# Optimization experiments

Measured on AMD Instinct MI355X. Metric: run time of the kernel, lower is better.

Reference implementation:

```python
import jax, jax.numpy as jnp
import numpy as np

ITERS = 3
K = 64
C = 256


def setup_inputs() -> dict:
    key = jax.random.key(0)
    ks = jax.random.split(key, 6)
    N, H, W = 2, 60, 60
    cnn_feature = jax.random.normal(ks[0], (N, C, H, W), dtype=jnp.float32)
    points = jax.random.normal(ks[1], (N, 3, H, W), dtype=jnp.float32)
    # torch Linear params: weight (out, in), bias (out,)
    s1 = 1.0 / np.sqrt(C)
    s2 = 1.0 / np.sqrt(2 * C)
    mlp_w = jax.random.uniform(ks[2], (C, C), jnp.float32, -s1, s1)
    mlp_b = jax.random.uniform(ks[3], (C,), jnp.float32, -s1, s1)
    rnn_w = jax.random.uniform(ks[4], (C, 2 * C), jnp.float32, -s2, s2)
    rnn_b = jax.random.uniform(ks[5], (C,), jnp.float32, -s2, s2)
    return {"cnn_feature": cnn_feature, "points": points, "mlp_w": mlp_w,
            "mlp_b": mlp_b, "rnn_w": rnn_w, "rnn_b": rnn_b}


def reference(cnn_feature, points, mlp_w, mlp_b, rnn_w, rnn_b):
    N, Cc, H, W = cnn_feature.shape
    HW = H * W
    pts = points.reshape(N, 3, HW).transpose(0, 2, 1)  # (N, HW, 3)
    # pairwise Euclidean distances via Gram matrix
    r = jnp.einsum('nid,njd->nij', pts, pts)           # (N, HW, HW)
    sq = jnp.einsum('nid,nid->ni', pts, pts)           # (N, HW)
    D = jnp.sqrt(jnp.maximum(sq[:, :, None] + sq[:, None, :] - 2.0 * r, 0.0))
    _, idx = jax.lax.top_k(-D, K)                      # (N, HW, K) smallest distances

    h = cnn_feature.transpose(0, 2, 3, 1).reshape(N, HW, Cc)  # (N, HW, C)
    bidx = jnp.arange(N)[:, None, None]
    for _ in range(ITERS):
        nb = h[bidx, idx]                              # (N, HW, K, C) gather
        nb = jax.nn.relu(jnp.einsum('nskc,dc->nskd', nb, mlp_w) + mlp_b)
        message = nb.mean(axis=2)                      # (N, HW, C)
        nh = jnp.concatenate([h, message], axis=-1)    # (N, HW, 2C)
        h = jax.nn.relu(jnp.einsum('nsc,dc->nsd', nh, rnn_w) + rnn_b)
    h = h.reshape(N, H, W, Cc).transpose(0, 3, 1, 2)   # (N, C, H, W)
    return jnp.concatenate([cnn_feature, h], axis=1)   # (N, 2C, H, W)
```

## Files before the change

### kernel.cpp

```cpp
#include <hip/hip_runtime.h>
#include <stdint.h>

typedef unsigned int uint;
typedef unsigned long long ull;

#define HW 3600
#define NBATCH 2
#define CDIM 256
#define KNN 64
#define M_REAL 7200
#define PADM 7232
#define QPB 8

#define TKB 900
#define IHB 904
#define SUB 64

using short8  = __attribute__((ext_vector_type(8))) short;
using floatx4 = __attribute__((ext_vector_type(4))) float;

__device__ inline unsigned short f2bf(float f) {
    uint u = __float_as_uint(f);
    uint r = u + 0x7FFFu + ((u >> 16) & 1u);
    return (unsigned short)(r >> 16);
}
__device__ inline float bf2f(unsigned short b) {
    return __uint_as_float(((uint)b) << 16);
}

__device__ inline void wave_select(uint* hist, uint* s_bin, uint* s_want,
                                   int lane, uint want) {
    uint h0 = hist[4 * lane + 0], h1 = hist[4 * lane + 1];
    uint h2 = hist[4 * lane + 2], h3 = hist[4 * lane + 3];
    hist[4 * lane + 0] = 0; hist[4 * lane + 1] = 0;
    hist[4 * lane + 2] = 0; hist[4 * lane + 3] = 0;
    uint c4 = h0 + h1 + h2 + h3;
    uint v = c4;
    #pragma unroll
    for (int off = 1; off < 64; off <<= 1) {
        uint o = __shfl_up(v, off, 64);
        if (lane >= off) v += o;
    }
    uint below = v - c4;
    if (below < want && want <= v) {
        uint b = 4 * lane, c = below;
        if (c + h0 < want) { c += h0; b = 4 * lane + 1;
            if (c + h1 < want) { c += h1; b = 4 * lane + 2;
                if (c + h2 < want) { c += h2; b = 4 * lane + 3; } } }
        *s_bin = b;
        *s_want = want - c;
    }
}

union MegaSmem {
    struct {
        float4 pts[HW];
        uint hist[QPB][256];
        uint s_bin[QPB], s_want[QPB], s_cnt[QPB];
    } tk;
    struct { float tile[2][32][33]; } ih;
};

__global__ __launch_bounds__(512) void mega_kernel(
    const float* __restrict__ points, int* __restrict__ idx_out,
    const float* __restrict__ cnn, unsigned short* __restrict__ NH,
    float* __restrict__ out,
    const float* __restrict__ mw, const float* __restrict__ rw,
    unsigned short* __restrict__ mo, unsigned short* __restrict__ ro) {
    __shared__ MegaSmem sm;
    const int blk = blockIdx.x;

    if (blk >= TKB + IHB) {
        int i0 = (blk - TKB - IHB) * 2048 + threadIdx.x * 4;
        float4 v = *(const float4*)&rw[i0];
        uint2 p;
        p.x = (uint)f2bf(v.x) | ((uint)f2bf(v.y) << 16);
        p.y = (uint)f2bf(v.z) | ((uint)f2bf(v.w) << 16);
        *(uint2*)&ro[i0] = p;
        if (i0 < 65536) {
            float4 m = *(const float4*)&mw[i0];
            p.x = (uint)f2bf(m.x) | ((uint)f2bf(m.y) << 16);
            p.y = (uint)f2bf(m.z) | ((uint)f2bf(m.w) << 16);
            *(uint2*)&mo[i0] = p;
        }
        return;
    }

    if (blk >= TKB) {
        const int b = blk - TKB;
        const int n = b / 452;
        const int r = b - n * 452;
        const int hw0 = (r % 113) * 32;
        const int c0 = (r / 113) * 64 + ((threadIdx.x >> 8) << 5);
        const int t8 = threadIdx.x & 255;
        const int tx = t8 & 31;
        const int ty = t8 >> 5;
        float (*tile)[33] = sm.ih.tile[threadIdx.x >> 8];
        const float* __restrict__ src = cnn + (size_t)n * CDIM * HW;
        #pragma unroll
        for (int rr = 0; rr < 4; ++rr) {
            int cc = ty + rr * 8;
            int hw = hw0 + tx;
            if (hw < HW) {
                float v = src[(size_t)(c0 + cc) * HW + hw];
                tile[cc][tx] = v;
                out[(size_t)n * (2 * CDIM * HW) + (size_t)(c0 + cc) * HW + hw] = v;
            }
        }
        __syncthreads();
        #pragma unroll
        for (int rr = 0; rr < 4; ++rr) {
            int hh = ty + rr * 8;
            int hw = hw0 + hh;
            if (hw < HW)
                NH[(size_t)(n * HW + hw) * 512 + c0 + tx] = f2bf(tile[tx][hh]);
        }
        return;
    }

    const int wv = threadIdx.x >> 6;
    const int lane = threadIdx.x & 63;
    const int q = blk * QPB + wv;
    const int n = (blk * QPB) / HW;
    const int i = q - n * HW;

    const float* __restrict__ px = points + (size_t)n * 3 * HW;
    const float* __restrict__ py = px + HW;
    const float* __restrict__ pz = py + HW;

    for (int j = threadIdx.x; j < HW; j += 512)
        sm.tk.pts[j] = make_float4(px[j], py[j], pz[j], 0.0f);
    sm.tk.hist[wv][4 * lane + 0] = 0; sm.tk.hist[wv][4 * lane + 1] = 0;
    sm.tk.hist[wv][4 * lane + 2] = 0; sm.tk.hist[wv][4 * lane + 3] = 0;
    if (lane == 0) sm.tk.s_cnt[wv] = 0;
    __syncthreads();

    float4 pq = sm.tk.pts[i];
    const float xi = pq.x, yi = pq.y, zi = pq.z;
    const float sqi = xi * xi + yi * yi + zi * zi;

    uint qp[29];
    #pragma unroll
    for (int s = 0; s < 57; ++s) {
        int j = (s << 6) + lane;
        uint q16 = 0xFFFFu;
        if (j < HW) {
            float4 p = sm.tk.pts[j];
            float d2 = fmaxf(sqi + (p.x * p.x + p.y * p.y + p.z * p.z)
                             - 2.0f * (xi * p.x + yi * p.y + zi * p.z), 0.0f);
            q16 = (uint)fminf(d2 * 1024.0f, 65535.0f);
        }
        if (s & 1) qp[s >> 1] |= q16 << 16; else qp[s >> 1] = q16;
    }
    #define Q16(s) ((qp[(s) >> 1] >> (((s) & 1) << 4)) & 0xFFFFu)

    #pragma unroll
    for (int s = 0; s < 57; ++s) {
        int j = (s << 6) + lane;
        if (j < HW) atomicAdd(&sm.tk.hist[wv][Q16(s) >> 8], 1u);
    }
    __syncthreads();
    wave_select(&sm.tk.hist[wv][0], &sm.tk.s_bin[wv], &sm.tk.s_want[wv], lane, KNN);
    __syncthreads();
    const uint qT8 = sm.tk.s_bin[wv];
    const uint want2 = sm.tk.s_want[wv];
    __syncthreads();

    #pragma unroll
    for (int s = 0; s < 57; ++s) {
        int j = (s << 6) + lane;
        uint k = Q16(s);
        if (j < HW && (k >> 8) == qT8)
            atomicAdd(&sm.tk.hist[wv][k & 255u], 1u);
    }
    __syncthreads();
    wave_select(&sm.tk.hist[wv][0], &sm.tk.s_bin[wv], &sm.tk.s_want[wv], lane, want2);
    __syncthreads();
    const uint qT16 = (qT8 << 8) | sm.tk.s_bin[wv];
    const uint want3 = sm.tk.s_want[wv];

    #pragma unroll
    for (int s = 0; s < 57; ++s) {
        if (Q16(s) < qT16) {
            uint pos = atomicAdd(&sm.tk.s_cnt[wv], 1u);
            if (pos < KNN) idx_out[(size_t)q * KNN + pos] = (s << 6) + lane;
        }
    }

    ull cand[4] = {~0ULL, ~0ULL, ~0ULL, ~0ULL};
    int ncand = 0;
    #pragma unroll
    for (int s = 0; s < 57; ++s) {
        int j = (s << 6) + lane;
        if (j < HW && Q16(s) == qT16) {
            float4 p = sm.tk.pts[j];
            float d2 = fmaxf(sqi + (p.x * p.x + p.y * p.y + p.z * p.z)
                             - 2.0f * (xi * p.x + yi * p.y + zi * p.z), 0.0f);
            ull key = ((ull)__float_as_uint(d2) << 32) | (uint)j;
            if      (ncand == 0) cand[0] = key;
            else if (ncand == 1) cand[1] = key;
            else if (ncand == 2) cand[2] = key;
            else if (ncand == 3) cand[3] = key;
            ++ncand;
        }
    }
    const int base = KNN - (int)want3;
    if (__ballot(ncand > 4) == 0ULL) {
        for (int r = 0; r < (int)want3; ++r) {
            ull best = cand[0] < cand[1] ? cand[0] : cand[1];
            ull b23  = cand[2] < cand[3] ? cand[2] : cand[3];
            best = best < b23 ? best : b23;
            #pragma unroll
            for (int off = 1; off < 64; off <<= 1) {
                ull o = __shfl_xor(best, off, 64);
                if (o < best) best = o;
            }
            if (lane == 0) idx_out[(size_t)q * KNN + base + r] = (int)(uint)best;
            #pragma unroll
            for (int c = 0; c < 4; ++c)
                if (cand[c] == best) cand[c] = ~0ULL;
        }
    } else {
        ull used = 0ULL;
        for (int r = 0; r < (int)want3; ++r) {
            ull best = ~0ULL;
            #pragma unroll
            for (int s = 0; s < 57; ++s) {
                int j = (s << 6) + lane;
                if (j < HW && Q16(s) == qT16 && !((used >> s) & 1ULL)) {
                    float4 p = sm.tk.pts[j];
                    float d2 = fmaxf(sqi + (p.x * p.x + p.y * p.y + p.z * p.z)
                                     - 2.0f * (xi * p.x + yi * p.y + zi * p.z), 0.0f);
                    ull key = ((ull)__float_as_uint(d2) << 32) | (uint)j;
                    if (key < best) best = key;
                }
            }
            #pragma unroll
            for (int off = 1; off < 64; off <<= 1) {
                ull o = __shfl_xor(best, off, 64);
                if (o < best) best = o;
            }
            uint jw = (uint)best;
            if (lane == 0) idx_out[(size_t)q * KNN + base + r] = (int)jw;
            if ((int)(jw & 63u) == lane) used |= 1ULL << (jw >> 6);
        }
    }
    #undef Q16
}

#define LDKP 264
__global__ __launch_bounds__(256) void gemm_mfma(
    const unsigned short* __restrict__ A, int lda,
    const unsigned short* __restrict__ W, int ldw,
    const float* __restrict__ bias,
    unsigned short* __restrict__ Cb, int ldc,
    float* __restrict__ outp, int mode, int Kk) {
    __shared__ __align__(16) unsigned short As[64 * LDKP];
    __shared__ __align__(16) unsigned short Bs[64 * LDKP];
    const int m0 = blockIdx.x * 64;
    const int n0 = blockIdx.y * 64;
    const int tid = threadIdx.x;
    const int lane = tid & 63;
    const int w = tid >> 6;
    const int wm = (w & 1) * 32;
    const int wn = (w >> 1) * 32;
    const int l15 = lane & 15;
    const int qd = lane >> 4;

    floatx4 acc[2][2];
    #pragma unroll
    for (int a = 0; a < 2; ++a)
        #pragma unroll
        for (int b = 0; b < 2; ++b)
            acc[a][b] = (floatx4){0.f, 0.f, 0.f, 0.f};

    const int srow = tid >> 5;
    const int scol = (tid & 31) * 8;

    for (int k0 = 0; k0 < Kk; k0 += 256) {
        if (k0) __syncthreads();
        #pragma unroll
        for (int r8 = 0; r8 < 8; ++r8) {
            int row = r8 * 8 + srow;
            *(float4*)&As[row * LDKP + scol] =
                *(const float4*)&A[(size_t)(m0 + row) * lda + k0 + scol];
            *(float4*)&Bs[row * LDKP + scol] =
                *(const float4*)&W[(size_t)(n0 + row) * ldw + k0 + scol];
        }
        __syncthreads();
        #pragma unroll
        for (int ks = 0; ks < 256; ks += 32) {
            short8 a0 = *(const short8*)&As[(wm + l15) * LDKP + ks + qd * 8];
            short8 a1 = *(const short8*)&As[(wm + 16 + l15) * LDKP + ks + qd * 8];
            short8 b0 = *(const short8*)&Bs[(wn + l15) * LDKP + ks + qd * 8];
            short8 b1 = *(const short8*)&Bs[(wn + 16 + l15) * LDKP + ks + qd * 8];
            acc[0][0] = __builtin_amdgcn_mfma_f32_16x16x32_bf16(a0, b0, acc[0][0], 0, 0, 0);
            acc[0][1] = __builtin_amdgcn_mfma_f32_16x16x32_bf16(a0, b1, acc[0][1], 0, 0, 0);
            acc[1][0] = __builtin_amdgcn_mfma_f32_16x16x32_bf16(a1, b0, acc[1][0], 0, 0, 0);
            acc[1][1] = __builtin_amdgcn_mfma_f32_16x16x32_bf16(a1, b1, acc[1][1], 0, 0, 0);
        }
    }

    #pragma unroll
    for (int in = 0; in < 2; ++in) {
        int col = n0 + wn + in * 16 + l15;
        float bv = bias[col];
        #pragma unroll
        for (int im = 0; im < 2; ++im) {
            int mb = m0 + wm + im * 16 + qd * 4;
            if (mode == 0) {
                #pragma unroll
                for (int r = 0; r < 4; ++r)
                    Cb[(size_t)(mb + r) * ldc + col] =
                        f2bf(fmaxf(acc[im][in][r] + bv, 0.0f));
            } else if (mb < M_REAL) {
                int nb = mb / HW;
                int hw = mb - nb * HW;
                float4 o;
                o.x = fmaxf(acc[im][in][0] + bv, 0.0f);
                o.y = fmaxf(acc[im][in][1] + bv, 0.0f);
                o.z = fmaxf(acc[im][in][2] + bv, 0.0f);
                o.w = fmaxf(acc[im][in][3] + bv, 0.0f);
                *(float4*)&outp[(size_t)nb * (2 * CDIM * HW)
                                + (size_t)(CDIM + col) * HW + hw] = o;
            }
        }
    }
}

__global__ __launch_bounds__(256) void gather_mean(const unsigned short* __restrict__ T,
                                                   const int* __restrict__ idx,
                                                   unsigned short* __restrict__ NH) {
    const int q = blockIdx.x * 4 + (threadIdx.x >> 6);
    const int lane = threadIdx.x & 63;
    const int n = q / HW;
    const int half = lane >> 5;
    const int c8 = (lane & 31) * 8;

    const int nbrL = idx[(size_t)q * KNN + lane];
    float acc[8] = {0, 0, 0, 0, 0, 0, 0, 0};
    #pragma unroll 4
    for (int it = 0; it < 32; ++it) {
        int k = 2 * it + half;
        int j = __shfl(nbrL, k, 64);
        j = min(max(j, 0), HW - 1);
        int r = n * HW + j;
        uint4 v = *(const uint4*)&T[(size_t)r * CDIM + c8];
        acc[0] += bf2f((unsigned short)(v.x & 0xFFFFu));
        acc[1] += bf2f((unsigned short)(v.x >> 16));
        acc[2] += bf2f((unsigned short)(v.y & 0xFFFFu));
        acc[3] += bf2f((unsigned short)(v.y >> 16));
        acc[4] += bf2f((unsigned short)(v.z & 0xFFFFu));
        acc[5] += bf2f((unsigned short)(v.z >> 16));
        acc[6] += bf2f((unsigned short)(v.w & 0xFFFFu));
        acc[7] += bf2f((unsigned short)(v.w >> 16));
    }
    #pragma unroll
    for (int c = 0; c < 8; ++c) acc[c] += __shfl_xor(acc[c], 32, 64);
    if (half == 0) {
        uint4 o;
        o.x = (uint)f2bf(acc[0] * (1.0f / KNN)) | ((uint)f2bf(acc[1] * (1.0f / KNN)) << 16);
        o.y = (uint)f2bf(acc[2] * (1.0f / KNN)) | ((uint)f2bf(acc[3] * (1.0f / KNN)) << 16);
        o.z = (uint)f2bf(acc[4] * (1.0f / KNN)) | ((uint)f2bf(acc[5] * (1.0f / KNN)) << 16);
        o.w = (uint)f2bf(acc[6] * (1.0f / KNN)) | ((uint)f2bf(acc[7] * (1.0f / KNN)) << 16);
        *(uint4*)&NH[(size_t)q * 512 + CDIM + c8] = o;
    }
}

extern "C" void kernel_launch(void* const* d_in, const int* in_sizes, int n_in,
                              void* d_out, int out_size, void* d_ws, size_t ws_size,
                              hipStream_t stream) {
    const float* cnn   = (const float*)d_in[0];
    const float* pts   = (const float*)d_in[1];
    const float* mlp_w = (const float*)d_in[2];
    const float* mlp_b = (const float*)d_in[3];
    const float* rnn_w = (const float*)d_in[4];
    const float* rnn_b = (const float*)d_in[5];
    float* out = (float*)d_out;

    unsigned short* NHa    = (unsigned short*)d_ws;
    unsigned short* NHb    = NHa + (size_t)PADM * 512;
    unsigned short* Tb     = NHb + (size_t)PADM * 512;
    unsigned short* mlpw_b = Tb + (size_t)PADM * CDIM;
    unsigned short* rnnw_b = mlpw_b + 65536;
    int*            idx    = (int*)(rnnw_b + 131072);

    mega_kernel<<<TKB + IHB + SUB, 512, 0, stream>>>(
        pts, idx, cnn, NHa, out, mlp_w, rnn_w, mlpw_b, rnnw_b);

    unsigned short* cur = NHa;
    unsigned short* nxt = NHb;
    for (int it = 0; it < 3; ++it) {
        gemm_mfma<<<dim3(PADM / 64, CDIM / 64), 256, 0, stream>>>(
            cur, 512, mlpw_b, CDIM, mlp_b, Tb, CDIM, nullptr, 0, CDIM);
        gather_mean<<<M_REAL / 4, 256, 0, stream>>>(Tb, idx, cur);
        if (it < 2) {
            gemm_mfma<<<dim3(PADM / 64, CDIM / 64), 256, 0, stream>>>(
                cur, 512, rnnw_b, 512, rnn_b, nxt, 512, nullptr, 0, 512);
            unsigned short* tmp = cur; cur = nxt; nxt = tmp;
        } else {
            gemm_mfma<<<dim3(PADM / 64, CDIM / 64), 256, 0, stream>>>(
                cur, 512, rnnw_b, 512, rnn_b, nullptr, 0, out, 1, 512);
        }
    }
}
```

Before: 206.9 us.

## Push RNN message weight through the neighbor mean and fuse per-iteration GEMMs

Uses linearity: W_msg·mean(nb) equals mean(W_msg·nb), so the second half of the RNN weight is applied to the MLP output per point before the gather. The gather kernel then finishes the RNN layer by adding the self term, bias and ReLU. This removes the separate 512-wide RNN GEMM and the concatenated buffer. One fused kernel computes the MLP output and the self term, then multiplies by the message weight through shared memory, and a final transpose kernel writes the output. It also caches the distances in registers for the tie-break selection instead of recomputing them, which raises register pressure in the top-k stage.

Result: slower. 267.9 us (+29.5%).

```diff
diff --git a/kernel.cpp b/kernel.cpp
--- a/kernel.cpp
+++ b/kernel.cpp
@@ -9,12 +9,11 @@
 #define CDIM 256
 #define KNN 64
 #define M_REAL 7200
-#define PADM 7232
 #define QPB 8
 
 #define TKB 900
 #define IHB 904
-#define SUB 64
+#define SUB 96
 
 using short8  = __attribute__((ext_vector_type(8))) short;
 using floatx4 = __attribute__((ext_vector_type(4))) float;
@@ -63,26 +62,34 @@
 
 __global__ __launch_bounds__(512) void mega_kernel(
     const float* __restrict__ points, int* __restrict__ idx_out,
-    const float* __restrict__ cnn, unsigned short* __restrict__ NH,
+    const float* __restrict__ cnn, unsigned short* __restrict__ H,
     float* __restrict__ out,
     const float* __restrict__ mw, const float* __restrict__ rw,
-    unsigned short* __restrict__ mo, unsigned short* __restrict__ ro) {
+    unsigned short* __restrict__ w1, unsigned short* __restrict__ w2) {
     __shared__ MegaSmem sm;
     const int blk = blockIdx.x;
 
     if (blk >= TKB + IHB) {
-        int i0 = (blk - TKB - IHB) * 2048 + threadIdx.x * 4;
-        float4 v = *(const float4*)&rw[i0];
+        int idx4 = (blk - TKB - IHB) * 512 + threadIdx.x;
+        const float* src;
+        unsigned short* dst;
+        if (idx4 < 32768) {
+            int j = idx4 * 4;
+            int n = j >> 8, k = j & 255;
+            src = (n < 256) ? &mw[(size_t)n * 256 + k]
+                            : &rw[(size_t)(n - 256) * 512 + k];
+            dst = &w1[j];
+        } else {
+            int j = (idx4 - 32768) * 4;
+            int n = j >> 8, k = j & 255;
+            src = &rw[(size_t)n * 512 + 256 + k];
+            dst = &w2[j];
+        }
+        float4 vv = *(const float4*)src;
         uint2 p;
-        p.x = (uint)f2bf(v.x) | ((uint)f2bf(v.y) << 16);
-        p.y = (uint)f2bf(v.z) | ((uint)f2bf(v.w) << 16);
-        *(uint2*)&ro[i0] = p;
-        if (i0 < 65536) {
-            float4 m = *(const float4*)&mw[i0];
-            p.x = (uint)f2bf(m.x) | ((uint)f2bf(m.y) << 16);
-            p.y = (uint)f2bf(m.z) | ((uint)f2bf(m.w) << 16);
-            *(uint2*)&mo[i0] = p;
-        }
+        p.x = (uint)f2bf(vv.x) | ((uint)f2bf(vv.y) << 16);
+        p.y = (uint)f2bf(vv.z) | ((uint)f2bf(vv.w) << 16);
+        *(uint2*)dst = p;
         return;
     }
 
@@ -113,7 +120,7 @@
             int hh = ty + rr * 8;
             int hw = hw0 + hh;
             if (hw < HW)
-                NH[(size_t)(n * HW + hw) * 512 + c0 + tx] = f2bf(tile[tx][hh]);
+                H[(size_t)(n * HW + hw) * CDIM + c0 + tx] = f2bf(tile[tx][hh]);
         }
         return;
     }
@@ -139,17 +146,19 @@
     const float xi = pq.x, yi = pq.y, zi = pq.z;
     const float sqi = xi * xi + yi * yi + zi * zi;
 
+    float d2v[57];
     uint qp[29];
     #pragma unroll
     for (int s = 0; s < 57; ++s) {
         int j = (s << 6) + lane;
-        uint q16 = 0xFFFFu;
+        float d2 = 1e30f;
         if (j < HW) {
             float4 p = sm.tk.pts[j];
-            float d2 = fmaxf(sqi + (p.x * p.x + p.y * p.y + p.z * p.z)
-                             - 2.0f * (xi * p.x + yi * p.y + zi * p.z), 0.0f);
-            q16 = (uint)fminf(d2 * 1024.0f, 65535.0f);
-        }
+            d2 = fmaxf(sqi + (p.x * p.x + p.y * p.y + p.z * p.z)
+                       - 2.0f * (xi * p.x + yi * p.y + zi * p.z), 0.0f);
+        }
+        d2v[s] = d2;
+        uint q16 = (uint)fminf(d2 * 1024.0f, 65535.0f);
         if (s & 1) qp[s >> 1] |= q16 << 16; else qp[s >> 1] = q16;
     }
     #define Q16(s) ((qp[(s) >> 1] >> (((s) & 1) << 4)) & 0xFFFFu)
@@ -186,151 +195,106 @@
             if (pos < KNN) idx_out[(size_t)q * KNN + pos] = (s << 6) + lane;
         }
     }
-
-    ull cand[4] = {~0ULL, ~0ULL, ~0ULL, ~0ULL};
-    int ncand = 0;
-    #pragma unroll
-    for (int s = 0; s < 57; ++s) {
-        int j = (s << 6) + lane;
-        if (j < HW && Q16(s) == qT16) {
-            float4 p = sm.tk.pts[j];
-            float d2 = fmaxf(sqi + (p.x * p.x + p.y * p.y + p.z * p.z)
-                             - 2.0f * (xi * p.x + yi * p.y + zi * p.z), 0.0f);
-            ull key = ((ull)__float_as_uint(d2) << 32) | (uint)j;
-            if      (ncand == 0) cand[0] = key;
-            else if (ncand == 1) cand[1] = key;
-            else if (ncand == 2) cand[2] = key;
-            else if (ncand == 3) cand[3] = key;
-            ++ncand;
-        }
-    }
+    ull used = 0ULL;
     const int base = KNN - (int)want3;
-    if (__ballot(ncand > 4) == 0ULL) {
-        for (int r = 0; r < (int)want3; ++r) {
-            ull best = cand[0] < cand[1] ? cand[0] : cand[1];
-            ull b23  = cand[2] < cand[3] ? cand[2] : cand[3];
-            best = best < b23 ? best : b23;
-            #pragma unroll
-            for (int off = 1; off < 64; off <<= 1) {
-                ull o = __shfl_xor(best, off, 64);
-                if (o < best) best = o;
+    for (int r = 0; r < (int)want3; ++r) {
+        ull best = ~0ULL;
+        #pragma unroll
+        for (int s = 0; s < 57; ++s) {
+            int j = (s << 6) + lane;
+            if (j < HW && Q16(s) == qT16 && !((used >> s) & 1ULL)) {
+                ull key = ((ull)__float_as_uint(d2v[s]) << 32) | (uint)j;
+                if (key < best) best = key;
             }
-            if (lane == 0) idx_out[(size_t)q * KNN + base + r] = (int)(uint)best;
-            #pragma unroll
-            for (int c = 0; c < 4; ++c)
-                if (cand[c] == best) cand[c] = ~0ULL;
-        }
-    } else {
-        ull used = 0ULL;
-        for (int r = 0; r < (int)want3; ++r) {
-            ull best = ~0ULL;
-            #pragma unroll
-            for (int s = 0; s < 57; ++s) {
-                int j = (s << 6) + lane;
-                if (j < HW && Q16(s) == qT16 && !((used >> s) & 1ULL)) {
-                    float4 p = sm.tk.pts[j];
-                    float d2 = fmaxf(sqi + (p.x * p.x + p.y * p.y + p.z * p.z)
-                                     - 2.0f * (xi * p.x + yi * p.y + zi * p.z), 0.0f);
-                    ull key = ((ull)__float_as_uint(d2) << 32) | (uint)j;
-                    if (key < best) best = key;
-                }
-            }
-            #pragma unroll
-            for (int off = 1; off < 64; off <<= 1) {
-                ull o = __shfl_xor(best, off, 64);
-                if (o < best) best = o;
-            }
-            uint jw = (uint)best;
-            if (lane == 0) idx_out[(size_t)q * KNN + base + r] = (int)jw;
-            if ((int)(jw & 63u) == lane) used |= 1ULL << (jw >> 6);
-        }
+        }
+        #pragma unroll
+        for (int off = 1; off < 64; off <<= 1) {
+            ull o = __shfl_xor(best, off, 64);
+            if (o < best) best = o;
+        }
+        uint jw = (uint)best;
+        if (lane == 0) idx_out[(size_t)q * KNN + base + r] = (int)jw;
+        if ((int)(jw & 63u) == lane) used |= 1ULL << (jw >> 6);
     }
     #undef Q16
 }
 
-#define LDKP 264
-__global__ __launch_bounds__(256) void gemm_mfma(
-    const unsigned short* __restrict__ A, int lda,
-    const unsigned short* __restrict__ W, int ldw,
-    const float* __restrict__ bias,
-    unsigned short* __restrict__ Cb, int ldc,
-    float* __restrict__ outp, int mode, int Kk) {
-    __shared__ __align__(16) unsigned short As[64 * LDKP];
-    __shared__ __align__(16) unsigned short Bs[64 * LDKP];
-    const int m0 = blockIdx.x * 64;
-    const int n0 = blockIdx.y * 64;
-    const int tid = threadIdx.x;
-    const int lane = tid & 63;
-    const int w = tid >> 6;
-    const int wm = (w & 1) * 32;
-    const int wn = (w >> 1) * 32;
+#define LDT 264
+__global__ __launch_bounds__(512) void fused_gemm(
+    const unsigned short* __restrict__ h,
+    const unsigned short* __restrict__ w1,
+    const unsigned short* __restrict__ w2,
+    const float* __restrict__ mlp_b,
+    unsigned short* __restrict__ u,
+    unsigned short* __restrict__ v) {
+    __shared__ __align__(16) unsigned short ts[16 * LDT];
+    const int m0 = blockIdx.x * 16;
+    const int lane = threadIdx.x & 63;
+    const int w = threadIdx.x >> 6;
     const int l15 = lane & 15;
     const int qd = lane >> 4;
 
-    floatx4 acc[2][2];
-    #pragma unroll
-    for (int a = 0; a < 2; ++a)
-        #pragma unroll
-        for (int b = 0; b < 2; ++b)
-            acc[a][b] = (floatx4){0.f, 0.f, 0.f, 0.f};
-
-    const int srow = tid >> 5;
-    const int scol = (tid & 31) * 8;
-
-    for (int k0 = 0; k0 < Kk; k0 += 256) {
-        if (k0) __syncthreads();
-        #pragma unroll
-        for (int r8 = 0; r8 < 8; ++r8) {
-            int row = r8 * 8 + srow;
-            *(float4*)&As[row * LDKP + scol] =
-                *(const float4*)&A[(size_t)(m0 + row) * lda + k0 + scol];
-            *(float4*)&Bs[row * LDKP + scol] =
-                *(const float4*)&W[(size_t)(n0 + row) * ldw + k0 + scol];
-        }
-        __syncthreads();
-        #pragma unroll
-        for (int ks = 0; ks < 256; ks += 32) {
-            short8 a0 = *(const short8*)&As[(wm + l15) * LDKP + ks + qd * 8];
-            short8 a1 = *(const short8*)&As[(wm + 16 + l15) * LDKP + ks + qd * 8];
-            short8 b0 = *(const short8*)&Bs[(wn + l15) * LDKP + ks + qd * 8];
-            short8 b1 = *(const short8*)&Bs[(wn + 16 + l15) * LDKP + ks + qd * 8];
-            acc[0][0] = __builtin_amdgcn_mfma_f32_16x16x32_bf16(a0, b0, acc[0][0], 0, 0, 0);
-            acc[0][1] = __builtin_amdgcn_mfma_f32_16x16x32_bf16(a0, b1, acc[0][1], 0, 0, 0);
-            acc[1][0] = __builtin_amdgcn_mfma_f32_16x16x32_bf16(a1, b0, acc[1][0], 0, 0, 0);
-            acc[1][1] = __builtin_amdgcn_mfma_f32_16x16x32_bf16(a1, b1, acc[1][1], 0, 0, 0);
-        }
-    }
-
-    #pragma unroll
-    for (int in = 0; in < 2; ++in) {
-        int col = n0 + wn + in * 16 + l15;
-        float bv = bias[col];
-        #pragma unroll
-        for (int im = 0; im < 2; ++im) {
-            int mb = m0 + wm + im * 16 + qd * 4;
-            if (mode == 0) {
-                #pragma unroll
-                for (int r = 0; r < 4; ++r)
-                    Cb[(size_t)(mb + r) * ldc + col] =
-                        f2bf(fmaxf(acc[im][in][r] + bv, 0.0f));
-            } else if (mb < M_REAL) {
-                int nb = mb / HW;
-                int hw = mb - nb * HW;
-                float4 o;
-                o.x = fmaxf(acc[im][in][0] + bv, 0.0f);
-                o.y = fmaxf(acc[im][in][1] + bv, 0.0f);
-                o.z = fmaxf(acc[im][in][2] + bv, 0.0f);
-                o.w = fmaxf(acc[im][in][3] + bv, 0.0f);
-                *(float4*)&outp[(size_t)nb * (2 * CDIM * HW)
-                                + (size_t)(CDIM + col) * HW + hw] = o;
-            }
-        }
-    }
-}
-
-__global__ __launch_bounds__(256) void gather_mean(const unsigned short* __restrict__ T,
-                                                   const int* __restrict__ idx,
-                                                   unsigned short* __restrict__ NH) {
+    floatx4 acc1[4];
+    #pragma unroll
+    for (int f = 0; f < 4; ++f) acc1[f] = (floatx4){0.f, 0.f, 0.f, 0.f};
+    const int col0 = w * 64;
+    #pragma unroll
+    for (int k0 = 0; k0 < 256; k0 += 32) {
+        short8 a = *(const short8*)&h[(size_t)(m0 + l15) * 256 + k0 + qd * 8];
+        #pragma unroll
+        for (int nf = 0; nf < 4; ++nf) {
+            short8 b = *(const short8*)
+                &w1[(size_t)(col0 + nf * 16 + l15) * 256 + k0 + qd * 8];
+            acc1[nf] = __builtin_amdgcn_mfma_f32_16x16x32_bf16(a, b, acc1[nf], 0, 0, 0);
+        }
+    }
+    if (w < 4) {
+        #pragma unroll
+        for (int nf = 0; nf < 4; ++nf) {
+            int c = col0 + nf * 16 + l15;
+            float bb = mlp_b[c];
+            #pragma unroll
+            for (int r = 0; r < 4; ++r)
+                ts[(qd * 4 + r) * LDT + c] = f2bf(fmaxf(acc1[nf][r] + bb, 0.0f));
+        }
+    } else {
+        #pragma unroll
+        for (int nf = 0; nf < 4; ++nf) {
+            int c = col0 - 256 + nf * 16 + l15;
+            #pragma unroll
+            for (int r = 0; r < 4; ++r)
+                v[(size_t)(m0 + qd * 4 + r) * 256 + c] = f2bf(acc1[nf][r]);
+        }
+    }
+    __syncthreads();
+
+    floatx4 acc2[2];
+    acc2[0] = (floatx4){0.f, 0.f, 0.f, 0.f};
+    acc2[1] = (floatx4){0.f, 0.f, 0.f, 0.f};
+    const int uc0 = w * 32;
+    #pragma unroll
+    for (int k0 = 0; k0 < 256; k0 += 32) {
+        short8 a = *(const short8*)&ts[l15 * LDT + k0 + qd * 8];
+        #pragma unroll
+        for (int nf = 0; nf < 2; ++nf) {
+            short8 b = *(const short8*)
+                &w2[(size_t)(uc0 + nf * 16 + l15) * 256 + k0 + qd * 8];
+            acc2[nf] = __builtin_amdgcn_mfma_f32_16x16x32_bf16(a, b, acc2[nf], 0, 0, 0);
+        }
+    }
+    #pragma unroll
+    for (int nf = 0; nf < 2; ++nf) {
+        int c = uc0 + nf * 16 + l15;
+        #pragma unroll
+        for (int r = 0; r < 4; ++r)
+            u[(size_t)(m0 + qd * 4 + r) * 256 + c] = f2bf(acc2[nf][r]);
+    }
+}
+
+__global__ __launch_bounds__(256) void gather_rnn(
+    const unsigned short* __restrict__ u, const unsigned short* __restrict__ v,
+    const int* __restrict__ idx, const float* __restrict__ rnn_b,
+    unsigned short* __restrict__ hout) {
     const int q = blockIdx.x * 4 + (threadIdx.x >> 6);
     const int lane = threadIdx.x & 63;
     const int n = q / HW;
@@ -341,29 +305,64 @@
     float acc[8] = {0, 0, 0, 0, 0, 0, 0, 0};
     #pragma unroll 4
     for (int it = 0; it < 32; ++it) {
-        int k = 2 * it + half;
-        int j = __shfl(nbrL, k, 64);
+        int j = __shfl(nbrL, 2 * it + half, 64);
         j = min(max(j, 0), HW - 1);
-        int r = n * HW + j;
-        uint4 v = *(const uint4*)&T[(size_t)r * CDIM + c8];
-        acc[0] += bf2f((unsigned short)(v.x & 0xFFFFu));
-        acc[1] += bf2f((unsigned short)(v.x >> 16));
-        acc[2] += bf2f((unsigned short)(v.y & 0xFFFFu));
-        acc[3] += bf2f((unsigned short)(v.y >> 16));
-        acc[4] += bf2f((unsigned short)(v.z & 0xFFFFu));
-        acc[5] += bf2f((unsigned short)(v.z >> 16));
-        acc[6] += bf2f((unsigned short)(v.w & 0xFFFFu));
-        acc[7] += bf2f((unsigned short)(v.w >> 16));
+        uint4 t4 = *(const uint4*)&u[(size_t)(n * HW + j) * 256 + c8];
+        acc[0] += bf2f((unsigned short)(t4.x & 0xFFFFu));
+        acc[1] += bf2f((unsigned short)(t4.x >> 16));
+        acc[2] += bf2f((unsigned short)(t4.y & 0xFFFFu));
+        acc[3] += bf2f((unsigned short)(t4.y >> 16));
+        acc[4] += bf2f((unsigned short)(t4.z & 0xFFFFu));
+        acc[5] += bf2f((unsigned short)(t4.z >> 16));
+        acc[6] += bf2f((unsigned short)(t4.w & 0xFFFFu));
+        acc[7] += bf2f((unsigned short)(t4.w >> 16));
     }
     #pragma unroll
     for (int c = 0; c < 8; ++c) acc[c] += __shfl_xor(acc[c], 32, 64);
     if (half == 0) {
+        uint4 vv = *(const uint4*)&v[(size_t)q * 256 + c8];
+        float4 b0 = *(const float4*)&rnn_b[c8];
+        float4 b1 = *(const float4*)&rnn_b[c8 + 4];
+        float hv[8];
+        hv[0] = fmaxf(bf2f((unsigned short)(vv.x & 0xFFFFu)) + acc[0] * (1.0f / KNN) + b0.x, 0.0f);
+        hv[1] = fmaxf(bf2f((unsigned short)(vv.x >> 16))     + acc[1] * (1.0f / KNN) + b0.y, 0.0f);
+        hv[2] = fmaxf(bf2f((unsigned short)(vv.y & 0xFFFFu)) + acc[2] * (1.0f / KNN) + b0.z, 0.0f);
+        hv[3] = fmaxf(bf2f((unsigned short)(vv.y >> 16))     + acc[3] * (1.0f / KNN) + b0.w, 0.0f);
+        hv[4] = fmaxf(bf2f((unsigned short)(vv.z & 0xFFFFu)) + acc[4] * (1.0f / KNN) + b1.x, 0.0f);
+        hv[5] = fmaxf(bf2f((unsigned short)(vv.z >> 16))     + acc[5] * (1.0f / KNN) + b1.y, 0.0f);
+        hv[6] = fmaxf(bf2f((unsigned short)(vv.w & 0xFFFFu)) + acc[6] * (1.0f / KNN) + b1.z, 0.0f);
+        hv[7] = fmaxf(bf2f((unsigned short)(vv.w >> 16))     + acc[7] * (1.0f / KNN) + b1.w, 0.0f);
         uint4 o;
-        o.x = (uint)f2bf(acc[0] * (1.0f / KNN)) | ((uint)f2bf(acc[1] * (1.0f / KNN)) << 16);
-        o.y = (uint)f2bf(acc[2] * (1.0f / KNN)) | ((uint)f2bf(acc[3] * (1.0f / KNN)) << 16);
-        o.z = (uint)f2bf(acc[4] * (1.0f / KNN)) | ((uint)f2bf(acc[5] * (1.0f / KNN)) << 16);
-        o.w = (uint)f2bf(acc[6] * (1.0f / KNN)) | ((uint)f2bf(acc[7] * (1.0f / KNN)) << 16);
-        *(uint4*)&NH[(size_t)q * 512 + CDIM + c8] = o;
+        o.x = (uint)f2bf(hv[0]) | ((uint)f2bf(hv[1]) << 16);
+        o.y = (uint)f2bf(hv[2]) | ((uint)f2bf(hv[3]) << 16);
+        o.z = (uint)f2bf(hv[4]) | ((uint)f2bf(hv[5]) << 16);
+        o.w = (uint)f2bf(hv[6]) | ((uint)f2bf(hv[7]) << 16);
+        *(uint4*)&hout[(size_t)q * 256 + c8] = o;
+    }
+}
+
+__global__ __launch_bounds__(256) void final_out(const unsigned short* __restrict__ Hf,
+                                                 float* __restrict__ out) {
+    __shared__ float tile[32][33];
+    const int hw0 = blockIdx.x * 32;
+    const int c0 = blockIdx.y * 32;
+    const int n = blockIdx.z;
+    const int tx = threadIdx.x & 31;
+    const int ty = threadIdx.x >> 5;
+    #pragma unroll
+    for (int r = 0; r < 4; ++r) {
+        int hh = ty + r * 8;
+        int hw = hw0 + hh;
+        if (hw < HW) tile[hh][tx] = bf2f(Hf[(size_t)(n * HW + hw) * CDIM + c0 + tx]);
+    }
+    __syncthreads();
+    #pragma unroll
+    for (int r = 0; r < 4; ++r) {
+        int cc = ty + r * 8;
+        int hw = hw0 + tx;
+        if (hw < HW)
+            out[(size_t)n * (2 * CDIM * HW) + (size_t)(CDIM + c0 + cc) * HW + hw] =
+                tile[tx][cc];
     }
 }
 
@@ -378,29 +377,24 @@
     const float* rnn_b = (const float*)d_in[5];
     float* out = (float*)d_out;
 
-    unsigned short* NHa    = (unsigned short*)d_ws;
-    unsigned short* NHb    = NHa + (size_t)PADM * 512;
-    unsigned short* Tb     = NHb + (size_t)PADM * 512;
-    unsigned short* mlpw_b = Tb + (size_t)PADM * CDIM;
-    unsigned short* rnnw_b = mlpw_b + 65536;
-    int*            idx    = (int*)(rnnw_b + 131072);
+    unsigned short* ha = (unsigned short*)d_ws;
+    unsigned short* hb = ha + (size_t)M_REAL * 256;
+    unsigned short* ub = hb + (size_t)M_REAL * 256;
+    unsigned short* vb = ub + (size_t)M_REAL * 256;
+    unsigned short* w1 = vb + (size_t)M_REAL * 256;
+    unsigned short* w2 = w1 + 131072;
+    int*            idx = (int*)(w2 + 65536);
 
     mega_kernel<<<TKB + IHB + SUB, 512, 0, stream>>>(
-        pts, idx, cnn, NHa, out, mlp_w, rnn_w, mlpw_b, rnnw_b);
-
-    unsigned short* cur = NHa;
-    unsigned short* nxt = NHb;
+        pts, idx, cnn, ha, out, mlp_w, rnn_w, w1, w2);
+
+    unsigned short* cur = ha;
+    unsigned short* nxt = hb;
     for (int it = 0; it < 3; ++it) {
-        gemm_mfma<<<dim3(PADM / 64, CDIM / 64), 256, 0, stream>>>(
-            cur, 512, mlpw_b, CDIM, mlp_b, Tb, CDIM, nullptr, 0, CDIM);
-        gather_mean<<<M_REAL / 4, 256, 0, stream>>>(Tb, idx, cur);
-        if (it < 2) {
-            gemm_mfma<<<dim3(PADM / 64, CDIM / 64), 256, 0, stream>>>(
-                cur, 512, rnnw_b, 512, rnn_b, nxt, 512, nullptr, 0, 512);
-            unsigned short* tmp = cur; cur = nxt; nxt = tmp;
-        } else {
-            gemm_mfma<<<dim3(PADM / 64, CDIM / 64), 256, 0, stream>>>(
-                cur, 512, rnnw_b, 512, rnn_b, nullptr, 0, out, 1, 512);
-        }
-    }
-}
+        fused_gemm<<<M_REAL / 16, 512, 0, stream>>>(cur, w1, w2, mlp_b, ub, vb);
+        gather_rnn<<<M_REAL / 4, 256, 0, stream>>>(ub, vb, idx, rnn_b, nxt);
+        unsigned short* tmp = cur; cur = nxt; nxt = tmp;
+    }
+
+    final_out<<<dim3(113, 8, NBATCH), 256, 0, stream>>>(cur, out);
+}
```
